# Performance work log

Measured on AMD Instinct MI355X. Metric: run time of the kernel, lower is better.

Reference implementation:

```python
import jax, jax.numpy as jnp
import numpy as np

B, D, R = 16384, 4096, 64       # batch tokens, embed_dim, low_rank_dimension
N_PART = 8                       # number of subspace partitions
P = R // N_PART                  # partition size = 8
N_SEL = 4                        # partitions selected per example


def setup_inputs() -> dict:
    key = jax.random.key(0)
    k1, k2, k3, k4 = jax.random.split(key, 4)
    base = jax.random.normal(k1, (B, D), dtype=jnp.float32)
    source = jax.random.normal(k2, (B, D), dtype=jnp.float32)
    # orthogonal low-rank rotation (torch.nn.utils.parametrizations.orthogonal)
    W, _ = jnp.linalg.qr(jax.random.normal(k3, (D, R), dtype=jnp.float32))  # [D, R], orthonormal cols
    subspaces = jax.random.randint(k4, (B, N_SEL), 0, N_PART)               # partition ids per example
    return {"base": base, "source": source, "W": W, "subspaces": subspaces}


def reference(base, source, W, subspaces):
    # rotate into low-rank space: [B, R]
    rotated_base = base @ W
    rotated_source = source @ W
    diff = rotated_source - rotated_base

    # per-example selected rotated-space indices (contiguous partitions of size P)
    # idx[b] = concat over selected partitions of [p*P, p*P+P)
    idx = (subspaces[:, :, None] * P + jnp.arange(P)).reshape(B, N_SEL * P)  # [B, N_SEL*P]

    # Selecting columns of diff and matching rows of W.T, then matmul, is
    # equivalent to masking unselected rotated dims to zero and doing one GEMM.
    mask = jnp.zeros((B, R), dtype=diff.dtype).at[jnp.arange(B)[:, None], idx].set(1.0)
    output = base + (diff * mask) @ W.T  # [B, D]
    return output.astype(base.dtype)
```

## Files before the change

### kernel.cpp

```cpp
#include <hip/hip_runtime.h>


#define D_DIM 4096
#define R_DIM 64
#define BM    32
#define WAVESTG 16384
#define OFF_RM  65536
#define SMEM_BYTES 70144

typedef short bf16vec8 __attribute__((ext_vector_type(8)));
typedef float f32x4v  __attribute__((ext_vector_type(4)));

__device__ __forceinline__ unsigned int f2bf_u(float f) {
  unsigned int u = __builtin_bit_cast(unsigned int, f);
  return (u + 0x7fffu + ((u >> 16) & 1u)) >> 16;
}
__device__ __forceinline__ unsigned int pack2bf(float a, float b) {
  return f2bf_u(a) | (f2bf_u(b) << 16);
}
__device__ __forceinline__ void async_ld16(const void* g, void* l) {
  __builtin_amdgcn_global_load_lds(
      (const __attribute__((address_space(1))) void*)g,
      (__attribute__((address_space(3))) void*)l, 16, 0, 0);
}

__global__ __launch_bounds__(256)
void lrri_prep(const float* __restrict__ W, unsigned short* __restrict__ Wt,
               unsigned short* __restrict__ Wb) {
  const int idx = blockIdx.x * blockDim.x + threadIdx.x;
  const int k = idx >> 4;
  const int j = (idx & 15) * 4;
  float4 w = *(const float4*)(W + (size_t)k * R_DIM + j);
  ushort4 p;
  p.x = (unsigned short)f2bf_u(w.x);
  p.y = (unsigned short)f2bf_u(w.y);
  p.z = (unsigned short)f2bf_u(w.z);
  p.w = (unsigned short)f2bf_u(w.w);
  *(ushort4*)(Wb + (size_t)k * R_DIM + j) = p;
  Wt[(size_t)(j + 0) * D_DIM + k] = p.x;
  Wt[(size_t)(j + 1) * D_DIM + k] = p.y;
  Wt[(size_t)(j + 2) * D_DIM + k] = p.z;
  Wt[(size_t)(j + 3) * D_DIM + k] = p.w;
}

template<bool USE_WS>
__global__ __launch_bounds__(256, 2)
void lrri_fused(const float* __restrict__ base, const float* __restrict__ srcp,
                const float* __restrict__ W, const int* __restrict__ subs,
                const unsigned short* __restrict__ Wt_bf,
                const unsigned short* __restrict__ Wb_bf,
                float* __restrict__ out)
{
  __shared__ __align__(16) unsigned char smem[SMEM_BYTES];
  const int tid  = threadIdx.x;
  const int wave = tid >> 6;
  const int lane = tid & 63;
  const int l4   = lane & 15;
  const int g    = lane >> 4;
  const int rh   = wave >> 1;
  const int kh   = wave & 1;
  const long rowbase = (long)blockIdx.x * BM;
  const long rowg    = rowbase + rh * 16;
  unsigned char* wbuf = smem + wave * WAVESTG;

  f32x4v acc[4];
  #pragma unroll
  for (int t = 0; t < 4; ++t) acc[t] = (f32x4v){0.f, 0.f, 0.f, 0.f};

  auto stage = [&](int p, int c) {
    const int kb = kh * 2048 + c * 64;
    unsigned char* buf = wbuf + p * 8192;
    #pragma unroll
    for (int i = 0; i < 4; ++i) {
      const int  r  = i * 4 + g;
      const unsigned cb = ((unsigned)(l4 * 16)) ^ ((unsigned)(r & 7) << 4);
      const long goff = (rowg + r) * (long)D_DIM + kb + (cb >> 2);
      async_ld16(base + goff, buf + i * 1024);
      async_ld16(srcp + goff, buf + 4096 + i * 1024);
    }
  };

  auto compute = [&](int p, int c) {
    const int kb = kh * 2048 + c * 64;
    const unsigned char* buf = wbuf + p * 8192;
    uint4 af[2];
    #pragma unroll
    for (int s = 0; s < 2; ++s) {
      const unsigned x = (unsigned)(l4 & 7) << 4;
      const unsigned cb0 = ((unsigned)(s * 128 + g * 32 +  0)) ^ x;
      const unsigned cb1 = ((unsigned)(s * 128 + g * 32 + 16)) ^ x;
      float4 fb0 = *(const float4*)(buf + l4 * 256 + cb0);
      float4 fb1 = *(const float4*)(buf + l4 * 256 + cb1);
      float4 fs0 = *(const float4*)(buf + 4096 + l4 * 256 + cb0);
      float4 fs1 = *(const float4*)(buf + 4096 + l4 * 256 + cb1);
      af[s].x = pack2bf(fs0.x - fb0.x, fs0.y - fb0.y);
      af[s].y = pack2bf(fs0.z - fb0.z, fs0.w - fb0.w);
      af[s].z = pack2bf(fs1.x - fb1.x, fs1.y - fb1.y);
      af[s].w = pack2bf(fs1.z - fb1.z, fs1.w - fb1.w);
    }
    #pragma unroll
    for (int t = 0; t < 4; ++t) {
      #pragma unroll
      for (int s = 0; s < 2; ++s) {
        uint4 bfrag;
        if (USE_WS) {
          bfrag = *(const uint4*)(Wt_bf + (size_t)(t * 16 + l4) * D_DIM +
                                  kb + s * 32 + g * 8);
        } else {
          unsigned int pq[4];
          #pragma unroll
          for (int e2 = 0; e2 < 4; ++e2) {
            float wa = W[(size_t)(kb + s * 32 + g * 8 + e2 * 2    ) * R_DIM + t * 16 + l4];
            float wb = W[(size_t)(kb + s * 32 + g * 8 + e2 * 2 + 1) * R_DIM + t * 16 + l4];
            pq[e2] = pack2bf(wa, wb);
          }
          bfrag.x = pq[0]; bfrag.y = pq[1]; bfrag.z = pq[2]; bfrag.w = pq[3];
        }
        acc[t] = __builtin_amdgcn_mfma_f32_16x16x32_bf16(
            __builtin_bit_cast(bf16vec8, af[s]),
            __builtin_bit_cast(bf16vec8, bfrag), acc[t], 0, 0, 0);
      }
    }
  };

  stage(0, 0);
  #pragma unroll 1
  for (int c = 0; c < 31; ++c) {
    stage((c + 1) & 1, c + 1);
    compute(c & 1, c);
  }
  compute(1, 31);

  {
    float* part = (float*)wbuf;
    #pragma unroll
    for (int t = 0; t < 4; ++t)
      #pragma unroll
      for (int i = 0; i < 4; ++i)
        part[(g * 4 + i) * 72 + t * 16 + l4] = acc[t][i];
  }
  __syncthreads();

  {
    const int row = tid >> 3, jg = tid & 7;
    const int lr  = row & 15;
    const float* pa = (const float*)(smem + ((row >> 4) * 2 + 0) * WAVESTG);
    const float* pb = (const float*)(smem + ((row >> 4) * 2 + 1) * WAVESTG);
    int4 sb = *(const int4*)(subs + (rowbase + row) * 4);
    unsigned mbits = (1u << sb.x) | (1u << sb.y) | (1u << sb.z) | (1u << sb.w);
    unsigned short v[8];
    #pragma unroll
    for (int jj = 0; jj < 8; ++jj) {
      const int j = jg * 8 + jj;
      float sum = pa[lr * 72 + j] + pb[lr * 72 + j];
      v[jj] = ((mbits >> (j >> 3)) & 1u) ? (unsigned short)f2bf_u(sum)
                                         : (unsigned short)0;
    }
    uint4 pk;
    pk.x = (unsigned)v[0] | ((unsigned)v[1] << 16);
    pk.y = (unsigned)v[2] | ((unsigned)v[3] << 16);
    pk.z = (unsigned)v[4] | ((unsigned)v[5] << 16);
    pk.w = (unsigned)v[6] | ((unsigned)v[7] << 16);
    *(uint4*)(smem + OFF_RM + row * 144 + jg * 16) = pk;
  }
  __syncthreads();

  uint4 a2[2][2];
  #pragma unroll
  for (int m = 0; m < 2; ++m)
    #pragma unroll
    for (int s = 0; s < 2; ++s)
      a2[m][s] = *(const uint4*)(smem + OFF_RM + (m * 16 + l4) * 144 +
                                 s * 64 + g * 16);
  float* cbuf = (float*)wbuf;
  #pragma unroll 1
  for (int grp = 0; grp < 16; ++grp) {
    const int cbase = wave * 1024 + grp * 64;
    float4 bb[8];
    #pragma unroll
    for (int v2 = 0; v2 < 8; ++v2) {
      const int r = g + v2 * 4;
      bb[v2] = *(const float4*)(base + (rowbase + r) * D_DIM + cbase + l4 * 4);
    }
    f32x4v a[2][4];
    #pragma unroll
    for (int m = 0; m < 2; ++m)
      #pragma unroll
      for (int t = 0; t < 4; ++t) a[m][t] = (f32x4v){0.f, 0.f, 0.f, 0.f};
    #pragma unroll
    for (int t = 0; t < 4; ++t) {
      #pragma unroll
      for (int s = 0; s < 2; ++s) {
        uint4 bfrag;
        if (USE_WS) {
          bfrag = *(const uint4*)(Wb_bf + (size_t)(cbase + t * 16 + l4) * R_DIM +
                                  s * 32 + g * 8);
        } else {
          const float* wp = W + (size_t)(cbase + t * 16 + l4) * R_DIM + s * 32 + g * 8;
          float4 wa = *(const float4*)(wp);
          float4 wb2 = *(const float4*)(wp + 4);
          bfrag.x = pack2bf(wa.x, wa.y); bfrag.y = pack2bf(wa.z, wa.w);
          bfrag.z = pack2bf(wb2.x, wb2.y); bfrag.w = pack2bf(wb2.z, wb2.w);
        }
        #pragma unroll
        for (int m = 0; m < 2; ++m)
          a[m][t] = __builtin_amdgcn_mfma_f32_16x16x32_bf16(
              __builtin_bit_cast(bf16vec8, a2[m][s]),
              __builtin_bit_cast(bf16vec8, bfrag), a[m][t], 0, 0, 0);
      }
    }
    #pragma unroll
    for (int m = 0; m < 2; ++m)
      #pragma unroll
      for (int t = 0; t < 4; ++t)
        #pragma unroll
        for (int i = 0; i < 4; ++i)
          cbuf[(m * 16 + g * 4 + i) * 72 + t * 16 + l4] = a[m][t][i];
    #pragma unroll
    for (int v2 = 0; v2 < 8; ++v2) {
      const int r = g + v2 * 4;
      f32x4v cv = *(const f32x4v*)(cbuf + r * 72 + l4 * 4);
      float4 o;
      o.x = cv[0] + bb[v2].x;
      o.y = cv[1] + bb[v2].y;
      o.z = cv[2] + bb[v2].z;
      o.w = cv[3] + bb[v2].w;
      *(float4*)(out + (rowbase + r) * D_DIM + cbase + l4 * 4) = o;
    }
  }
}

extern "C" void kernel_launch(void* const* d_in, const int* in_sizes, int n_in,
                              void* d_out, int out_size, void* d_ws, size_t ws_size,
                              hipStream_t stream) {
  const float* base = (const float*)d_in[0];
  const float* srcp = (const float*)d_in[1];
  const float* W    = (const float*)d_in[2];
  const int*   subs = (const int*)d_in[3];
  float* out = (float*)d_out;

  const int nblocks = 16384 / BM;
  const size_t wbytes = (size_t)2 * R_DIM * D_DIM * sizeof(unsigned short);
  if (d_ws && ws_size >= wbytes) {
    unsigned short* Wt = (unsigned short*)d_ws;
    unsigned short* Wb = Wt + (size_t)R_DIM * D_DIM;
    lrri_prep<<<256, 256, 0, stream>>>(W, Wt, Wb);
    lrri_fused<true><<<nblocks, 256, 0, stream>>>(base, srcp, W, subs, Wt, Wb, out);
  } else {
    lrri_fused<false><<<nblocks, 256, 0, stream>>>(base, srcp, W, subs, nullptr, nullptr, out);
  }
}
```

Baseline: 252.3 us.

## Restructure fused kernel to single-wave blocks of eight rows with triple-buffered staging

Switches from 256-thread blocks handling 32 rows (split across waves by K-half) to 64-thread single-wave blocks handling 8 rows over the full K. Each wave streams base/source through a 3-deep LDS ring using async loads and explicit vmcnt waits. W fragments are prefetched into registers with inline-asm global loads, and the cross-wave reduction and barriers are removed. The cost is that only half of each 16-row MFMA tile carries useful rows, so matrix work per useful row roughly doubles. W must also be re-read per 8 rows instead of per 32 rows.

```diff
diff --git a/kernel.cpp b/kernel.cpp
--- a/kernel.cpp
+++ b/kernel.cpp
@@ -3,13 +3,21 @@
 
 #define D_DIM 4096
 #define R_DIM 64
-#define BM    32
-#define WAVESTG 16384
-#define OFF_RM  65536
-#define SMEM_BYTES 70144
+#define ROWS  8
+#define NCH   64
 
 typedef short bf16vec8 __attribute__((ext_vector_type(8)));
 typedef float f32x4v  __attribute__((ext_vector_type(4)));
+typedef unsigned int u32x4 __attribute__((ext_vector_type(4)));
+
+#define OFF_RM      12288
+#define SMEM_BYTES  13440
+
+#define VMWAIT(N)                                              \
+  do {                                                         \
+    asm volatile("s_waitcnt vmcnt(" #N ")" ::: "memory");      \
+    __builtin_amdgcn_sched_barrier(0);                         \
+  } while (0)
 
 __device__ __forceinline__ unsigned int f2bf_u(float f) {
   unsigned int u = __builtin_bit_cast(unsigned int, f);
@@ -18,10 +26,10 @@
 __device__ __forceinline__ unsigned int pack2bf(float a, float b) {
   return f2bf_u(a) | (f2bf_u(b) << 16);
 }
-__device__ __forceinline__ void async_ld16(const void* g, void* l) {
+__device__ __forceinline__ void async_ld16(const void* gp, void* lp) {
   __builtin_amdgcn_global_load_lds(
-      (const __attribute__((address_space(1))) void*)g,
-      (__attribute__((address_space(3))) void*)l, 16, 0, 0);
+      (const __attribute__((address_space(1))) void*)gp,
+      (__attribute__((address_space(3))) void*)lp, 16, 0, 0);
 }
 
 __global__ __launch_bounds__(256)
@@ -44,7 +52,7 @@
 }
 
 template<bool USE_WS>
-__global__ __launch_bounds__(256, 2)
+__global__ __launch_bounds__(64)
 void lrri_fused(const float* __restrict__ base, const float* __restrict__ srcp,
                 const float* __restrict__ W, const int* __restrict__ subs,
                 const unsigned short* __restrict__ Wt_bf,
@@ -53,179 +61,199 @@
 {
   __shared__ __align__(16) unsigned char smem[SMEM_BYTES];
   const int tid  = threadIdx.x;
-  const int wave = tid >> 6;
-  const int lane = tid & 63;
-  const int l4   = lane & 15;
-  const int g    = lane >> 4;
-  const int rh   = wave >> 1;
-  const int kh   = wave & 1;
-  const long rowbase = (long)blockIdx.x * BM;
-  const long rowg    = rowbase + rh * 16;
-  unsigned char* wbuf = smem + wave * WAVESTG;
+  const int l4   = tid & 15;
+  const int g    = tid >> 4;
+  const long rowbase = (long)blockIdx.x * ROWS;
+
+  auto stage = [&](int c) {
+    unsigned char* buf = smem + (c % 3) * 4096;
+    const int kb = c * 64;
+    #pragma unroll
+    for (int i = 0; i < 2; ++i) {
+      const long goff = (rowbase + i * 4 + g) * (long)D_DIM + kb + l4 * 4;
+      async_ld16(base + goff, buf + i * 1024);
+    }
+    #pragma unroll
+    for (int i = 0; i < 2; ++i) {
+      const long goff = (rowbase + i * 4 + g) * (long)D_DIM + kb + l4 * 4;
+      async_ld16(srcp + goff, buf + 2048 + i * 1024);
+    }
+  };
+
+  auto wload = [&](u32x4 (&dst)[8], int kb) {
+    const char* wbp = (const char*)Wt_bf + (size_t)kb * 2 + l4 * 8192 + g * 16;
+    const char* a0 = wbp;
+    const char* a1 = wbp + 16 * 8192;
+    const char* a2 = wbp + 32 * 8192;
+    const char* a3 = wbp + 48 * 8192;
+    asm volatile(
+        "global_load_dwordx4 %0, %8, off\n\t"
+        "global_load_dwordx4 %1, %8, off offset:64\n\t"
+        "global_load_dwordx4 %2, %9, off\n\t"
+        "global_load_dwordx4 %3, %9, off offset:64\n\t"
+        "global_load_dwordx4 %4, %10, off\n\t"
+        "global_load_dwordx4 %5, %10, off offset:64\n\t"
+        "global_load_dwordx4 %6, %11, off\n\t"
+        "global_load_dwordx4 %7, %11, off offset:64"
+        : "=&v"(dst[0]), "=&v"(dst[1]), "=&v"(dst[2]), "=&v"(dst[3]),
+          "=&v"(dst[4]), "=&v"(dst[5]), "=&v"(dst[6]), "=&v"(dst[7])
+        : "v"(a0), "v"(a1), "v"(a2), "v"(a3)
+        : "memory");
+  };
 
   f32x4v acc[4];
   #pragma unroll
   for (int t = 0; t < 4; ++t) acc[t] = (f32x4v){0.f, 0.f, 0.f, 0.f};
 
-  auto stage = [&](int p, int c) {
-    const int kb = kh * 2048 + c * 64;
-    unsigned char* buf = wbuf + p * 8192;
-    #pragma unroll
-    for (int i = 0; i < 4; ++i) {
-      const int  r  = i * 4 + g;
-      const unsigned cb = ((unsigned)(l4 * 16)) ^ ((unsigned)(r & 7) << 4);
-      const long goff = (rowg + r) * (long)D_DIM + kb + (cb >> 2);
-      async_ld16(base + goff, buf + i * 1024);
-      async_ld16(srcp + goff, buf + 4096 + i * 1024);
-    }
-  };
-
-  auto compute = [&](int p, int c) {
-    const int kb = kh * 2048 + c * 64;
-    const unsigned char* buf = wbuf + p * 8192;
-    uint4 af[2];
-    #pragma unroll
-    for (int s = 0; s < 2; ++s) {
-      const unsigned x = (unsigned)(l4 & 7) << 4;
-      const unsigned cb0 = ((unsigned)(s * 128 + g * 32 +  0)) ^ x;
-      const unsigned cb1 = ((unsigned)(s * 128 + g * 32 + 16)) ^ x;
-      float4 fb0 = *(const float4*)(buf + l4 * 256 + cb0);
-      float4 fb1 = *(const float4*)(buf + l4 * 256 + cb1);
-      float4 fs0 = *(const float4*)(buf + 4096 + l4 * 256 + cb0);
-      float4 fs1 = *(const float4*)(buf + 4096 + l4 * 256 + cb1);
-      af[s].x = pack2bf(fs0.x - fb0.x, fs0.y - fb0.y);
-      af[s].y = pack2bf(fs0.z - fb0.z, fs0.w - fb0.w);
-      af[s].z = pack2bf(fs1.x - fb1.x, fs1.y - fb1.y);
-      af[s].w = pack2bf(fs1.z - fb1.z, fs1.w - fb1.w);
-    }
-    #pragma unroll
-    for (int t = 0; t < 4; ++t) {
+  auto ph1_compute = [&](int c, const u32x4 (&wf)[8]) {
+    const unsigned char* buf = smem + (c % 3) * 4096;
+    u32x4 af[2] = {{0u,0u,0u,0u},{0u,0u,0u,0u}};
+    if (l4 < ROWS) {
       #pragma unroll
       for (int s = 0; s < 2; ++s) {
-        uint4 bfrag;
-        if (USE_WS) {
-          bfrag = *(const uint4*)(Wt_bf + (size_t)(t * 16 + l4) * D_DIM +
-                                  kb + s * 32 + g * 8);
-        } else {
-          unsigned int pq[4];
-          #pragma unroll
-          for (int e2 = 0; e2 < 4; ++e2) {
-            float wa = W[(size_t)(kb + s * 32 + g * 8 + e2 * 2    ) * R_DIM + t * 16 + l4];
-            float wb = W[(size_t)(kb + s * 32 + g * 8 + e2 * 2 + 1) * R_DIM + t * 16 + l4];
-            pq[e2] = pack2bf(wa, wb);
-          }
-          bfrag.x = pq[0]; bfrag.y = pq[1]; bfrag.z = pq[2]; bfrag.w = pq[3];
-        }
+        const int bo = l4 * 256 + s * 128 + g * 32;
+        float4 fb0 = *(const float4*)(buf + bo);
+        float4 fb1 = *(const float4*)(buf + bo + 16);
+        float4 fs0 = *(const float4*)(buf + 2048 + bo);
+        float4 fs1 = *(const float4*)(buf + 2048 + bo + 16);
+        af[s].x = pack2bf(fs0.x - fb0.x, fs0.y - fb0.y);
+        af[s].y = pack2bf(fs0.z - fb0.z, fs0.w - fb0.w);
+        af[s].z = pack2bf(fs1.x - fb1.x, fs1.y - fb1.y);
+        af[s].w = pack2bf(fs1.z - fb1.z, fs1.w - fb1.w);
+      }
+    }
+    #pragma unroll
+    for (int t = 0; t < 4; ++t)
+      #pragma unroll
+      for (int s = 0; s < 2; ++s)
         acc[t] = __builtin_amdgcn_mfma_f32_16x16x32_bf16(
             __builtin_bit_cast(bf16vec8, af[s]),
-            __builtin_bit_cast(bf16vec8, bfrag), acc[t], 0, 0, 0);
-      }
-    }
+            __builtin_bit_cast(bf16vec8, wf[t * 2 + s]), acc[t], 0, 0, 0);
   };
 
-  stage(0, 0);
-  #pragma unroll 1
-  for (int c = 0; c < 31; ++c) {
-    stage((c + 1) & 1, c + 1);
-    compute(c & 1, c);
-  }
-  compute(1, 31);
-
-  {
-    float* part = (float*)wbuf;
-    #pragma unroll
-    for (int t = 0; t < 4; ++t)
-      #pragma unroll
-      for (int i = 0; i < 4; ++i)
-        part[(g * 4 + i) * 72 + t * 16 + l4] = acc[t][i];
-  }
-  __syncthreads();
-
-  {
-    const int row = tid >> 3, jg = tid & 7;
-    const int lr  = row & 15;
-    const float* pa = (const float*)(smem + ((row >> 4) * 2 + 0) * WAVESTG);
-    const float* pb = (const float*)(smem + ((row >> 4) * 2 + 1) * WAVESTG);
-    int4 sb = *(const int4*)(subs + (rowbase + row) * 4);
-    unsigned mbits = (1u << sb.x) | (1u << sb.y) | (1u << sb.z) | (1u << sb.w);
-    unsigned short v[8];
-    #pragma unroll
-    for (int jj = 0; jj < 8; ++jj) {
-      const int j = jg * 8 + jj;
-      float sum = pa[lr * 72 + j] + pb[lr * 72 + j];
-      v[jj] = ((mbits >> (j >> 3)) & 1u) ? (unsigned short)f2bf_u(sum)
-                                         : (unsigned short)0;
-    }
-    uint4 pk;
-    pk.x = (unsigned)v[0] | ((unsigned)v[1] << 16);
-    pk.y = (unsigned)v[2] | ((unsigned)v[3] << 16);
-    pk.z = (unsigned)v[4] | ((unsigned)v[5] << 16);
-    pk.w = (unsigned)v[6] | ((unsigned)v[7] << 16);
-    *(uint4*)(smem + OFF_RM + row * 144 + jg * 16) = pk;
-  }
-  __syncthreads();
-
-  uint4 a2[2][2];
-  #pragma unroll
-  for (int m = 0; m < 2; ++m)
-    #pragma unroll
-    for (int s = 0; s < 2; ++s)
-      a2[m][s] = *(const uint4*)(smem + OFF_RM + (m * 16 + l4) * 144 +
-                                 s * 64 + g * 16);
-  float* cbuf = (float*)wbuf;
-  #pragma unroll 1
-  for (int grp = 0; grp < 16; ++grp) {
-    const int cbase = wave * 1024 + grp * 64;
-    float4 bb[8];
-    #pragma unroll
-    for (int v2 = 0; v2 < 8; ++v2) {
-      const int r = g + v2 * 4;
-      bb[v2] = *(const float4*)(base + (rowbase + r) * D_DIM + cbase + l4 * 4);
-    }
-    f32x4v a[2][4];
-    #pragma unroll
-    for (int m = 0; m < 2; ++m)
-      #pragma unroll
-      for (int t = 0; t < 4; ++t) a[m][t] = (f32x4v){0.f, 0.f, 0.f, 0.f};
+  if constexpr (USE_WS) {
+    u32x4 wb0[8], wb1[8];
+    stage(0); wload(wb0, 0); stage(1); wload(wb1, 64);
+    #pragma unroll 1
+    for (int cc = 0; cc < 62; cc += 2) {
+      stage(cc + 2);
+      VMWAIT(16);
+      ph1_compute(cc, wb0);
+      wload(wb0, (cc + 2) * 64);
+      stage(cc + 3);
+      VMWAIT(16);
+      ph1_compute(cc + 1, wb1);
+      wload(wb1, (cc + 3) * 64);
+    }
+    VMWAIT(12);
+    ph1_compute(62, wb0);
+    VMWAIT(0);
+    ph1_compute(63, wb1);
+  } else {
+    #pragma unroll 1
+    for (int c = 0; c < NCH; ++c) {
+      stage(c);
+      VMWAIT(0);
+      u32x4 wf[8];
+      const int kb = c * 64;
+      #pragma unroll
+      for (int ts = 0; ts < 8; ++ts) {
+        const int t = ts >> 1, s = ts & 1;
+        unsigned int pq[4];
+        #pragma unroll
+        for (int e2 = 0; e2 < 4; ++e2) {
+          float wa = W[(size_t)(kb + s * 32 + g * 8 + e2 * 2    ) * R_DIM + t * 16 + l4];
+          float wb = W[(size_t)(kb + s * 32 + g * 8 + e2 * 2 + 1) * R_DIM + t * 16 + l4];
+          pq[e2] = pack2bf(wa, wb);
+        }
+        wf[ts].x = pq[0]; wf[ts].y = pq[1]; wf[ts].z = pq[2]; wf[ts].w = pq[3];
+      }
+      ph1_compute(c, wf);
+    }
+  }
+
+  if (g < 2) {
+    #pragma unroll
+    for (int i = 0; i < 4; ++i) {
+      const int row = g * 4 + i;
+      const int4 sb = *(const int4*)(subs + (size_t)(rowbase + row) * 4);
+      const unsigned mbits = (1u << sb.x) | (1u << sb.y) |
+                             (1u << sb.z) | (1u << sb.w);
+      #pragma unroll
+      for (int t = 0; t < 4; ++t) {
+        const int j = t * 16 + l4;
+        const unsigned short v = ((mbits >> (j >> 3)) & 1u)
+                                     ? (unsigned short)f2bf_u(acc[t][i])
+                                     : (unsigned short)0;
+        ((unsigned short*)(smem + OFF_RM))[row * 72 + j] = v;
+      }
+    }
+  }
+
+  uint4 a2[2] = {{0u,0u,0u,0u},{0u,0u,0u,0u}};
+  if (l4 < ROWS) {
+    a2[0] = *(const uint4*)(smem + OFF_RM + l4 * 144 + g * 16);
+    a2[1] = *(const uint4*)(smem + OFF_RM + l4 * 144 + 64 + g * 16);
+  }
+
+  #pragma unroll 2
+  for (int grp = 0; grp < 64; ++grp) {
+    const int cbase = grp * 64;
+    uint4 wb[8];
+    if (USE_WS) {
+      #pragma unroll
+      for (int ts = 0; ts < 8; ++ts) {
+        const int t = ts >> 1, s = ts & 1;
+        wb[ts] = *(const uint4*)(Wb_bf + (size_t)(cbase + t * 16 + l4) * R_DIM +
+                                 s * 32 + g * 8);
+      }
+    } else {
+      #pragma unroll
+      for (int ts = 0; ts < 8; ++ts) {
+        const int t = ts >> 1, s = ts & 1;
+        const float* wp = W + (size_t)(cbase + t * 16 + l4) * R_DIM + s * 32 + g * 8;
+        float4 wa = *(const float4*)(wp);
+        float4 wc = *(const float4*)(wp + 4);
+        wb[ts].x = pack2bf(wa.x, wa.y); wb[ts].y = pack2bf(wa.z, wa.w);
+        wb[ts].z = pack2bf(wc.x, wc.y); wb[ts].w = pack2bf(wc.z, wc.w);
+      }
+    }
+    float4 bb[2];
+    #pragma unroll
+    for (int i2 = 0; i2 < 2; ++i2) {
+      const int r = i2 * 4 + g;
+      bb[i2] = *(const float4*)(base + (rowbase + r) * (long)D_DIM + cbase + l4 * 4);
+    }
+    f32x4v a[4];
+    #pragma unroll
+    for (int t = 0; t < 4; ++t) a[t] = (f32x4v){0.f, 0.f, 0.f, 0.f};
     #pragma unroll
     for (int t = 0; t < 4; ++t) {
       #pragma unroll
       for (int s = 0; s < 2; ++s) {
-        uint4 bfrag;
-        if (USE_WS) {
-          bfrag = *(const uint4*)(Wb_bf + (size_t)(cbase + t * 16 + l4) * R_DIM +
-                                  s * 32 + g * 8);
-        } else {
-          const float* wp = W + (size_t)(cbase + t * 16 + l4) * R_DIM + s * 32 + g * 8;
-          float4 wa = *(const float4*)(wp);
-          float4 wb2 = *(const float4*)(wp + 4);
-          bfrag.x = pack2bf(wa.x, wa.y); bfrag.y = pack2bf(wa.z, wa.w);
-          bfrag.z = pack2bf(wb2.x, wb2.y); bfrag.w = pack2bf(wb2.z, wb2.w);
-        }
-        #pragma unroll
-        for (int m = 0; m < 2; ++m)
-          a[m][t] = __builtin_amdgcn_mfma_f32_16x16x32_bf16(
-              __builtin_bit_cast(bf16vec8, a2[m][s]),
-              __builtin_bit_cast(bf16vec8, bfrag), a[m][t], 0, 0, 0);
-      }
-    }
-    #pragma unroll
-    for (int m = 0; m < 2; ++m)
+        a[t] = __builtin_amdgcn_mfma_f32_16x16x32_bf16(
+            __builtin_bit_cast(bf16vec8, a2[s]),
+            __builtin_bit_cast(bf16vec8, wb[t * 2 + s]), a[t], 0, 0, 0);
+      }
+    }
+    float* cbuf = (float*)(smem + (grp & 1) * 4096);
+    if (g < 2) {
       #pragma unroll
       for (int t = 0; t < 4; ++t)
         #pragma unroll
         for (int i = 0; i < 4; ++i)
-          cbuf[(m * 16 + g * 4 + i) * 72 + t * 16 + l4] = a[m][t][i];
-    #pragma unroll
-    for (int v2 = 0; v2 < 8; ++v2) {
-      const int r = g + v2 * 4;
+          cbuf[(g * 4 + i) * 72 + t * 16 + l4] = a[t][i];
+    }
+    #pragma unroll
+    for (int i2 = 0; i2 < 2; ++i2) {
+      const int r = i2 * 4 + g;
       f32x4v cv = *(const f32x4v*)(cbuf + r * 72 + l4 * 4);
       float4 o;
-      o.x = cv[0] + bb[v2].x;
-      o.y = cv[1] + bb[v2].y;
-      o.z = cv[2] + bb[v2].z;
-      o.w = cv[3] + bb[v2].w;
-      *(float4*)(out + (rowbase + r) * D_DIM + cbase + l4 * 4) = o;
+      o.x = cv[0] + bb[i2].x;
+      o.y = cv[1] + bb[i2].y;
+      o.z = cv[2] + bb[i2].z;
+      o.w = cv[3] + bb[i2].w;
+      *(float4*)(out + (rowbase + r) * (long)D_DIM + cbase + l4 * 4) = o;
     }
   }
 }
@@ -239,14 +267,14 @@
   const int*   subs = (const int*)d_in[3];
   float* out = (float*)d_out;
 
-  const int nblocks = 16384 / BM;
+  const int nblocks = 16384 / ROWS;
   const size_t wbytes = (size_t)2 * R_DIM * D_DIM * sizeof(unsigned short);
   if (d_ws && ws_size >= wbytes) {
     unsigned short* Wt = (unsigned short*)d_ws;
     unsigned short* Wb = Wt + (size_t)R_DIM * D_DIM;
     lrri_prep<<<256, 256, 0, stream>>>(W, Wt, Wb);
-    lrri_fused<true><<<nblocks, 256, 0, stream>>>(base, srcp, W, subs, Wt, Wb, out);
+    lrri_fused<true><<<nblocks, 64, 0, stream>>>(base, srcp, W, subs, Wt, Wb, out);
   } else {
-    lrri_fused<false><<<nblocks, 256, 0, stream>>>(base, srcp, W, subs, nullptr, nullptr, out);
-  }
-}
+    lrri_fused<false><<<nblocks, 64, 0, stream>>>(base, srcp, W, subs, nullptr, nullptr, out);
+  }
+}
```

After: 345.3 us. +36.9%, slower.
